# Kernel tuning notes

Measured on AMD Instinct MI355X. Metric: run time of the kernel, lower is better.

The kernel has to match this reference:

```python
import jax, jax.numpy as jnp
import numpy as np

N_NODES = 100000
N_EDGES = 3200000
N_GRAPHS = 1024
HID = 64
NUM_CLASSES = 21


def setup_inputs() -> dict:
    key = jax.random.key(0)
    ks = jax.random.split(key, 12)
    x = jax.random.normal(ks[0], (N_NODES, 1), dtype=jnp.float32)
    edge_index = jax.random.randint(ks[1], (2, N_EDGES), 0, N_NODES, dtype=jnp.int64)
    batch = jnp.sort(jax.random.randint(ks[2], (N_NODES,), 0, N_GRAPHS, dtype=jnp.int64))
    def lin(k, fan_in, fan_out):
        bound = 1.0 / np.sqrt(fan_in)
        return jax.random.uniform(k, (fan_in, fan_out), jnp.float32, -bound, bound)
    return {
        "x": x,
        "edge_index": edge_index,
        "batch": batch,
        # SAGEConv1: lin_l (on aggregated neighbors, with bias), lin_r (root, no bias)
        "W1l": lin(ks[3], 1, HID), "b1": jnp.zeros((HID,), jnp.float32), "W1r": lin(ks[4], 1, HID),
        # SAGEConv2
        "W2l": lin(ks[5], HID, HID), "b2": jnp.zeros((HID,), jnp.float32), "W2r": lin(ks[6], HID, HID),
        # classifier
        "Wc": lin(ks[7], HID, NUM_CLASSES), "bc": jnp.zeros((NUM_CLASSES,), jnp.float32),
    }


def _sage_conv(x, src, dst, Wl, bl, Wr):
    # mean-aggregate neighbor features: gather from src, scatter-mean to dst
    msg = x[src]                                              # [E, F] gather
    agg = jax.ops.segment_sum(msg, dst, num_segments=N_NODES)  # [N, F]
    cnt = jax.ops.segment_sum(jnp.ones((src.shape[0],), x.dtype), dst, num_segments=N_NODES)
    agg = agg / jnp.maximum(cnt, 1.0)[:, None]
    # out = lin_l(aggr) + lin_r(x)
    return agg @ Wl + bl + x @ Wr


def reference(x, edge_index, batch, W1l, b1, W1r, W2l, b2, W2r, Wc, bc):
    src, dst = edge_index[0], edge_index[1]
    h = jax.nn.relu(_sage_conv(x, src, dst, W1l, b1, W1r))
    h = jax.nn.relu(_sage_conv(h, src, dst, W2l, b2, W2r))
    # global mean pool over graphs
    pooled = jax.ops.segment_sum(h, batch, num_segments=N_GRAPHS)
    gcnt = jax.ops.segment_sum(jnp.ones((h.shape[0],), h.dtype), batch, num_segments=N_GRAPHS)
    pooled = pooled / jnp.maximum(gcnt, 1.0)[:, None]
    return pooled @ Wc + bc
```

## Files before the change

### kernel.cpp

```cpp
#include <hip/hip_runtime.h>

#define N_NODES 100000
#define N_EDGES 3200000
#define N_GRAPHS 1024
#define NCLS 21
#define NBKT 782
#define CAP 4480
#define NB 512
#define CHUNK 6250
#define TROW 72

typedef short s8v __attribute__((ext_vector_type(8)));
typedef float f4v __attribute__((ext_vector_type(4)));
typedef float f2v __attribute__((ext_vector_type(2)));

__device__ __forceinline__ float bf2f(unsigned short u) {
    return __uint_as_float(((unsigned)u) << 16);
}
__device__ __forceinline__ unsigned short f2bf(float f) {
    unsigned u = __float_as_uint(f);
    unsigned r = 0x7fffu + ((u >> 16) & 1u);
    return (unsigned short)((u + r) >> 16);
}
__device__ __forceinline__ f2v up2(unsigned w) {
    f2v r;
    r.x = __uint_as_float(w << 16);
    r.y = __uint_as_float(w & 0xffff0000u);
    return r;
}

__global__ void k_prep(const float* __restrict__ W2l, const float* __restrict__ W2r,
                       unsigned short* __restrict__ wp,
                       const int* __restrict__ batch, int* __restrict__ gstart,
                       int* __restrict__ gcur) {
    if (blockIdx.x < 32) {
        int tid = blockIdx.x * 256 + threadIdx.x;
        int frag = tid >> 9;
        int r = tid & 511;
        int L = r >> 3, j = r & 7;
        int kstep = frag >> 2, nt = frag & 3;
        int k = kstep * 32 + (L >> 4) * 8 + j;
        int n = nt * 16 + (L & 15);
        float val = (k < 64) ? W2l[k * 64 + n] : W2r[(k - 64) * 64 + n];
        wp[tid] = f2bf(val);
    } else if (blockIdx.x < 37) {
        int g = (blockIdx.x - 32) * 256 + threadIdx.x;
        if (g > N_GRAPHS) return;
        if (g == N_GRAPHS) { gstart[N_GRAPHS] = N_NODES; return; }
        int lo = 0, hi = N_NODES;
        while (lo < hi) { int m = (lo + hi) >> 1; if (batch[m] < g) lo = m + 1; else hi = m; }
        gstart[g] = lo;
    } else {
        for (int i = threadIdx.x; i < NBKT; i += 256) gcur[i] = i * CAP;
    }
}

__global__ __launch_bounds__(256) void k_binone(const int* __restrict__ src,
                                                const int* __restrict__ dst,
                                                int* __restrict__ gcur,
                                                unsigned int* __restrict__ bins) {
    __shared__ unsigned int ebuf[CHUNK];
    __shared__ unsigned short bbuf[CHUNK];
    __shared__ int lh[NBKT];
    __shared__ int lbase[NBKT];
    int t = threadIdx.x;
    for (int i = t; i < NBKT; i += 256) lh[i] = 0;
    __syncthreads();
    const int2* s2 = (const int2*)(src + blockIdx.x * CHUNK);
    const int2* d2 = (const int2*)(dst + blockIdx.x * CHUNK);
    for (int i = t; i < CHUNK / 2; i += 256) {
        int2 s = s2[i];
        int2 d = d2[i];
        uint2 pp;
        pp.x = ((unsigned)s.x << 7) | (unsigned)(d.x & 127);
        pp.y = ((unsigned)s.y << 7) | (unsigned)(d.y & 127);
        *(uint2*)(&ebuf[2 * i]) = pp;
        bbuf[2 * i]     = (unsigned short)(d.x >> 7);
        bbuf[2 * i + 1] = (unsigned short)(d.y >> 7);
        atomicAdd(&lh[d.x >> 7], 1);
        atomicAdd(&lh[d.y >> 7], 1);
    }
    __syncthreads();
    for (int i = t; i < NBKT; i += 256)
        lbase[i] = atomicAdd(&gcur[i], lh[i]);
    __syncthreads();
    for (int i = t; i < NBKT; i += 256) lh[i] = lbase[i];
    __syncthreads();
    for (int i = t; i < CHUNK; i += 256) {
        int b = (int)bbuf[i];
        int pos = atomicAdd(&lh[b], 1);
        if (pos < (b + 1) * CAP) bins[pos] = ebuf[i];
    }
}

__global__ __launch_bounds__(256) void k_build(
    const int* __restrict__ gcur, unsigned int* __restrict__ bins,
    int* __restrict__ row, unsigned short* __restrict__ deg,
    const float* __restrict__ x,
    const float* __restrict__ W1l, const float* __restrict__ b1,
    const float* __restrict__ W1r, unsigned short* __restrict__ h1b) {
    __shared__ unsigned int ebuf[CAP];
    __shared__ int hist[128];
    __shared__ int curs[128];
    __shared__ int lds[128];
    __shared__ float t1[128];
    int k = blockIdx.x, t = threadIdx.x;
    int e0 = k * CAP;
    int cnt = min(gcur[k] - e0, CAP);
    if (t < 128) { hist[t] = 0; t1[t] = 0.0f; }
    __syncthreads();
    for (int i = t; i < cnt; i += 256) {
        unsigned p = bins[e0 + i];
        ebuf[i] = p;
        atomicAdd(&hist[p & 127u], 1);
    }
    __syncthreads();
    if (t < 128) lds[t] = hist[t];
    __syncthreads();
    for (int off = 1; off < 128; off <<= 1) {
        int cur = (t < 128) ? lds[t] : 0;
        int add = (t < 128 && t >= off) ? lds[t - off] : 0;
        __syncthreads();
        if (t < 128) lds[t] = cur + add;
        __syncthreads();
    }
    if (t < 128) {
        int run = e0 + lds[t] - hist[t];
        curs[t] = run;
        int n = k * 128 + t;
        if (n < N_NODES) { row[n] = run; deg[n] = (unsigned short)hist[t]; }
    }
    __syncthreads();
    for (int i = t; i < cnt; i += 256) {
        unsigned p = ebuf[i];
        int slot = (int)(p & 127u);
        int pos = atomicAdd(&curs[slot], 1);
        bins[pos] = p >> 7;
        atomicAdd(&t1[slot], x[p >> 7]);
    }
    __syncthreads();
    for (int i = t; i < 128 * 64; i += 256) {
        int slot = i >> 6, f = i & 63;
        int n = k * 128 + slot;
        if (n >= N_NODES) break;
        float a = t1[slot] / fmaxf((float)hist[slot], 1.0f);
        float v = a * W1l[f] + b1[f] + x[n] * W1r[f];
        h1b[(size_t)n * 64 + f] = f2bf(fmaxf(v, 0.0f));
    }
}

__global__ __launch_bounds__(256) void k_l2f(
    const int* __restrict__ row, const unsigned short* __restrict__ deg,
    const unsigned int* __restrict__ csr,
    const unsigned short* __restrict__ h1b,
    const unsigned short* __restrict__ wp, const float* __restrict__ b2,
    unsigned short* __restrict__ h2b) {
    __shared__ unsigned short tile[4][16 * TROW];
    int wid = threadIdx.x >> 6;
    int w = blockIdx.x * 4 + wid;
    if (w >= N_NODES / 16) return;
    int L = threadIdx.x & 63;
    int fo = L & 7;
    int g  = L >> 3;
    unsigned short* tw = tile[wid];

    int nA = w * 16 + g;
    int nB = nA + 8;
    int r0A = row[nA]; int dnA = (int)deg[nA];
    int r0B = row[nB]; int dnB = (int)deg[nB];

#define SWZ(v, j) __builtin_amdgcn_ds_swizzle((v), (((j) << 5) | 0x18))
#define GA(j, dj) { int sj = SWZ(idx, j); \
                    dj = *(const uint4*)(h1b + (size_t)(unsigned)sj * 64 + fo * 8); }
#define AC(dj) { p0 += up2(dj.x); p1 += up2(dj.y); p2 += up2(dj.z); p3 += up2(dj.w); }
#define REM(j) if ((j) < rem) { int sj = SWZ(idx, j); \
                    uint4 d = *(const uint4*)(h1b + (size_t)(unsigned)sj * 64 + fo * 8); \
                    AC(d) }

#pragma unroll
    for (int pass = 0; pass < 2; pass++) {
        int r0 = pass ? r0B : r0A;
        int dn = pass ? dnB : dnA;
        int trow = g + 8 * pass;
        int r1 = r0 + dn;
        f2v p0 = {0.f, 0.f}, p1 = p0, p2 = p0, p3 = p0;
        int base = r0;
        int idx = (int)csr[min(base + fo, r1 - 1)];
        while (base + 8 <= r1) {
            int nb = base + 8;
            int idxn = (int)csr[min(nb + fo, r1 - 1)];
            uint4 d0, d1, d2, d3, d4, d5, d6, d7;
            GA(0, d0) GA(1, d1) GA(2, d2) GA(3, d3)
            GA(4, d4) GA(5, d5) GA(6, d6) GA(7, d7)
            idx = idxn;
            AC(d0) AC(d1) AC(d2) AC(d3)
            AC(d4) AC(d5) AC(d6) AC(d7)
            base = nb;
        }
        int rem = r1 - base;
        if (rem > 0) {
            REM(0) REM(1) REM(2) REM(3)
            REM(4) REM(5) REM(6) REM(7)
        }
        float inv = 1.0f / fmaxf((float)dn, 1.0f);
        p0 *= inv; p1 *= inv; p2 *= inv; p3 *= inv;
        unsigned w0 = (unsigned)f2bf(p0.x) | ((unsigned)f2bf(p0.y) << 16);
        unsigned w1 = (unsigned)f2bf(p1.x) | ((unsigned)f2bf(p1.y) << 16);
        unsigned w2 = (unsigned)f2bf(p2.x) | ((unsigned)f2bf(p2.y) << 16);
        unsigned w3 = (unsigned)f2bf(p3.x) | ((unsigned)f2bf(p3.y) << 16);
        uint4 pk; pk.x = w0; pk.y = w1; pk.z = w2; pk.w = w3;
        *(uint4*)(tw + trow * TROW + fo * 8) = pk;
    }
#undef SWZ
#undef GA
#undef AC
#undef REM

    int m = L & 15, q = L >> 4;
    int nrow = w * 16 + m;

    const s8v a0 = *(const s8v*)(tw + m * TROW + q * 8);
    const s8v a1 = *(const s8v*)(tw + m * TROW + 32 + q * 8);
    const s8v a2 = *(const s8v*)(h1b + (size_t)nrow * 64 + q * 8);
    const s8v a3 = *(const s8v*)(h1b + (size_t)nrow * 64 + 32 + q * 8);

#define LOADB(i) s8v B##i = *(const s8v*)(wp + (i) * 512 + L * 8)
    LOADB(0); LOADB(1); LOADB(2); LOADB(3);
    LOADB(4); LOADB(5); LOADB(6); LOADB(7);
    LOADB(8); LOADB(9); LOADB(10); LOADB(11);
    LOADB(12); LOADB(13); LOADB(14); LOADB(15);
#undef LOADB

    f4v acc0 = {0.f, 0.f, 0.f, 0.f}, acc1 = acc0, acc2 = acc0, acc3 = acc0;
    acc0 = __builtin_amdgcn_mfma_f32_16x16x32_bf16(a0, B0,  acc0, 0, 0, 0);
    acc0 = __builtin_amdgcn_mfma_f32_16x16x32_bf16(a1, B4,  acc0, 0, 0, 0);
    acc0 = __builtin_amdgcn_mfma_f32_16x16x32_bf16(a2, B8,  acc0, 0, 0, 0);
    acc0 = __builtin_amdgcn_mfma_f32_16x16x32_bf16(a3, B12, acc0, 0, 0, 0);
    acc1 = __builtin_amdgcn_mfma_f32_16x16x32_bf16(a0, B1,  acc1, 0, 0, 0);
    acc1 = __builtin_amdgcn_mfma_f32_16x16x32_bf16(a1, B5,  acc1, 0, 0, 0);
    acc1 = __builtin_amdgcn_mfma_f32_16x16x32_bf16(a2, B9,  acc1, 0, 0, 0);
    acc1 = __builtin_amdgcn_mfma_f32_16x16x32_bf16(a3, B13, acc1, 0, 0, 0);
    acc2 = __builtin_amdgcn_mfma_f32_16x16x32_bf16(a0, B2,  acc2, 0, 0, 0);
    acc2 = __builtin_amdgcn_mfma_f32_16x16x32_bf16(a1, B6,  acc2, 0, 0, 0);
    acc2 = __builtin_amdgcn_mfma_f32_16x16x32_bf16(a2, B10, acc2, 0, 0, 0);
    acc2 = __builtin_amdgcn_mfma_f32_16x16x32_bf16(a3, B14, acc2, 0, 0, 0);
    acc3 = __builtin_amdgcn_mfma_f32_16x16x32_bf16(a0, B3,  acc3, 0, 0, 0);
    acc3 = __builtin_amdgcn_mfma_f32_16x16x32_bf16(a1, B7,  acc3, 0, 0, 0);
    acc3 = __builtin_amdgcn_mfma_f32_16x16x32_bf16(a2, B11, acc3, 0, 0, 0);
    acc3 = __builtin_amdgcn_mfma_f32_16x16x32_bf16(a3, B15, acc3, 0, 0, 0);

    int fcol = L & 15;
    float bia0 = b2[fcol], bia1 = b2[16 + fcol], bia2 = b2[32 + fcol], bia3 = b2[48 + fcol];
    int rbase = w * 16 + q * 4;
#pragma unroll
    for (int r = 0; r < 4; r++) {
        size_t o = (size_t)(rbase + r) * 64 + fcol;
        h2b[o]      = f2bf(fmaxf(acc0[r] + bia0, 0.0f));
        h2b[o + 16] = f2bf(fmaxf(acc1[r] + bia1, 0.0f));
        h2b[o + 32] = f2bf(fmaxf(acc2[r] + bia2, 0.0f));
        h2b[o + 48] = f2bf(fmaxf(acc3[r] + bia3, 0.0f));
    }
}

__global__ __launch_bounds__(256) void k_head(
    const unsigned short* __restrict__ h2b, const int* __restrict__ gstart,
    const float* __restrict__ Wc, const float* __restrict__ bc,
    float* __restrict__ out) {
    __shared__ float part[4][64];
    __shared__ float rowv[64];
    int g = blockIdx.x;
    int wid = threadIdx.x >> 6;
    int f = threadIdx.x & 63;
    int ns = gstart[g], ne = gstart[g + 1];
    float s = 0.0f;
    int n = ns + wid;
    for (; n + 12 < ne; n += 16) {
        float v0 = bf2f(h2b[(size_t)(n)      * 64 + f]);
        float v1 = bf2f(h2b[(size_t)(n + 4)  * 64 + f]);
        float v2 = bf2f(h2b[(size_t)(n + 8)  * 64 + f]);
        float v3 = bf2f(h2b[(size_t)(n + 12) * 64 + f]);
        s += (v0 + v1) + (v2 + v3);
    }
    for (; n < ne; n += 4) s += bf2f(h2b[(size_t)n * 64 + f]);
    part[wid][f] = s;
    __syncthreads();
    if (threadIdx.x < 64) {
        float tot = part[0][f] + part[1][f] + part[2][f] + part[3][f];
        rowv[f] = tot / fmaxf((float)(ne - ns), 1.0f);
    }
    __syncthreads();
    if (threadIdx.x < NCLS) {
        float acc = bc[threadIdx.x];
#pragma unroll
        for (int kk = 0; kk < 64; kk++) acc += rowv[kk] * Wc[kk * NCLS + threadIdx.x];
        out[g * NCLS + threadIdx.x] = acc;
    }
}

extern "C" void kernel_launch(void* const* d_in, const int* in_sizes, int n_in,
                              void* d_out, int out_size, void* d_ws, size_t ws_size,
                              hipStream_t stream) {
    const float* x     = (const float*)d_in[0];
    const int*   eidx  = (const int*)d_in[1];
    const int*   batch = (const int*)d_in[2];
    const float* W1l   = (const float*)d_in[3];
    const float* b1    = (const float*)d_in[4];
    const float* W1r   = (const float*)d_in[5];
    const float* W2l   = (const float*)d_in[6];
    const float* b2    = (const float*)d_in[7];
    const float* W2r   = (const float*)d_in[8];
    const float* Wc    = (const float*)d_in[9];
    const float* bc    = (const float*)d_in[10];
    float* out = (float*)d_out;

    const int* src = eidx;
    const int* dst = eidx + N_EDGES;

    char* p = (char*)d_ws;
    unsigned int* bins  = (unsigned int*)p;     p += (size_t)NBKT * CAP * 4;
    unsigned short* h1b = (unsigned short*)p;   p += (size_t)N_NODES * 64 * 2;
    unsigned short* h2b = (unsigned short*)p;   p += (size_t)N_NODES * 64 * 2;
    int* row   = (int*)p;                       p += (size_t)(N_NODES + 1) * 4;
    unsigned short* deg = (unsigned short*)p;   p += (size_t)N_NODES * 2;
    int* gcur  = (int*)p;                       p += NBKT * 4;
    int* gstart= (int*)p;                       p += (N_GRAPHS + 1) * 4;
    unsigned short* wp = (unsigned short*)p;    p += 8192 * 2;

    k_prep  <<<38, 256, 0, stream>>>(W2l, W2r, wp, batch, gstart, gcur);
    k_binone<<<NB, 256, 0, stream>>>(src, dst, gcur, bins);
    k_build <<<NBKT, 256, 0, stream>>>(gcur, bins, row, deg, x, W1l, b1, W1r, h1b);
    k_l2f   <<<(N_NODES / 16 + 3) / 4, 256, 0, stream>>>(row, deg, bins, h1b, wp, b2, h2b);
    k_head  <<<N_GRAPHS, 256, 0, stream>>>(h2b, gstart, Wc, bc, out);
}
```

Before: 234.1 us.

## Recompute layer-1 features on the fly from per-node scalars instead of gathering h1

Layer 1 has input dimension 1, so each h1 row is fully determined by two scalars: the mean neighbor x and the node's own x. k_build now stores only these as a float2 per node, and k_l2f rebuilds relu(a*W1l + x*W1r + b1) per edge in registers. The 128-byte bf16 gather per edge becomes an 8-byte gather plus about 64 FMAs and maxes per edge. Using fp32 inputs also drops one bf16 rounding before aggregation. The cost is much more ALU work per edge in exchange for far less gather traffic.

```diff
diff --git a/kernel.cpp b/kernel.cpp
--- a/kernel.cpp
+++ b/kernel.cpp
@@ -22,11 +22,8 @@
     unsigned r = 0x7fffu + ((u >> 16) & 1u);
     return (unsigned short)((u + r) >> 16);
 }
-__device__ __forceinline__ f2v up2(unsigned w) {
-    f2v r;
-    r.x = __uint_as_float(w << 16);
-    r.y = __uint_as_float(w & 0xffff0000u);
-    return r;
+__device__ __forceinline__ f2v max2(f2v v) {
+    f2v r; r.x = fmaxf(v.x, 0.0f); r.y = fmaxf(v.y, 0.0f); return r;
 }
 
 __global__ void k_prep(const float* __restrict__ W2l, const float* __restrict__ W2r,
@@ -96,9 +93,7 @@
 __global__ __launch_bounds__(256) void k_build(
     const int* __restrict__ gcur, unsigned int* __restrict__ bins,
     int* __restrict__ row, unsigned short* __restrict__ deg,
-    const float* __restrict__ x,
-    const float* __restrict__ W1l, const float* __restrict__ b1,
-    const float* __restrict__ W1r, unsigned short* __restrict__ h1b) {
+    const float* __restrict__ x, float2* __restrict__ ax) {
     __shared__ unsigned int ebuf[CAP];
     __shared__ int hist[128];
     __shared__ int curs[128];
@@ -139,20 +134,22 @@
         atomicAdd(&t1[slot], x[p >> 7]);
     }
     __syncthreads();
-    for (int i = t; i < 128 * 64; i += 256) {
-        int slot = i >> 6, f = i & 63;
-        int n = k * 128 + slot;
-        if (n >= N_NODES) break;
-        float a = t1[slot] / fmaxf((float)hist[slot], 1.0f);
-        float v = a * W1l[f] + b1[f] + x[n] * W1r[f];
-        h1b[(size_t)n * 64 + f] = f2bf(fmaxf(v, 0.0f));
+    if (t < 128) {
+        int n = k * 128 + t;
+        if (n < N_NODES) {
+            float a = t1[t] / fmaxf((float)hist[t], 1.0f);
+            float2 v; v.x = a; v.y = x[n];
+            ax[n] = v;
+        }
     }
 }
 
 __global__ __launch_bounds__(256) void k_l2f(
     const int* __restrict__ row, const unsigned short* __restrict__ deg,
     const unsigned int* __restrict__ csr,
-    const unsigned short* __restrict__ h1b,
+    const float2* __restrict__ ax,
+    const float* __restrict__ W1l, const float* __restrict__ b1,
+    const float* __restrict__ W1r,
     const unsigned short* __restrict__ wp, const float* __restrict__ b2,
     unsigned short* __restrict__ h2b) {
     __shared__ unsigned short tile[4][16 * TROW];
@@ -164,18 +161,32 @@
     int g  = L >> 3;
     unsigned short* tw = tile[wid];
 
+    f2v w1l_[4], w1r_[4], bb_[4];
+    {
+        const f2v* pl = (const f2v*)(W1l + fo * 8);
+        const f2v* pr = (const f2v*)(W1r + fo * 8);
+        const f2v* pb = (const f2v*)(b1  + fo * 8);
+#pragma unroll
+        for (int q = 0; q < 4; q++) { w1l_[q] = pl[q]; w1r_[q] = pr[q]; bb_[q] = pb[q]; }
+    }
+
     int nA = w * 16 + g;
     int nB = nA + 8;
     int r0A = row[nA]; int dnA = (int)deg[nA];
     int r0B = row[nB]; int dnB = (int)deg[nB];
 
 #define SWZ(v, j) __builtin_amdgcn_ds_swizzle((v), (((j) << 5) | 0x18))
-#define GA(j, dj) { int sj = SWZ(idx, j); \
-                    dj = *(const uint4*)(h1b + (size_t)(unsigned)sj * 64 + fo * 8); }
-#define AC(dj) { p0 += up2(dj.x); p1 += up2(dj.y); p2 += up2(dj.z); p3 += up2(dj.w); }
-#define REM(j) if ((j) < rem) { int sj = SWZ(idx, j); \
-                    uint4 d = *(const uint4*)(h1b + (size_t)(unsigned)sj * 64 + fo * 8); \
-                    AC(d) }
+#define EDGE(j) { \
+    unsigned au = (unsigned)SWZ((int)__float_as_uint(pr0.x), j); \
+    unsigned xu = (unsigned)SWZ((int)__float_as_uint(pr0.y), j); \
+    float a_ = __uint_as_float(au), x_ = __uint_as_float(xu); \
+    f2v av; av.x = a_; av.y = a_; \
+    f2v xv; xv.x = x_; xv.y = x_; \
+    pp0 += max2(av * w1l_[0] + (xv * w1r_[0] + bb_[0])); \
+    pp1 += max2(av * w1l_[1] + (xv * w1r_[1] + bb_[1])); \
+    pp2 += max2(av * w1l_[2] + (xv * w1r_[2] + bb_[2])); \
+    pp3 += max2(av * w1l_[3] + (xv * w1r_[3] + bb_[3])); }
+#define REM(j) if ((j) < rem) EDGE(j)
 
 #pragma unroll
     for (int pass = 0; pass < 2; pass++) {
@@ -183,19 +194,20 @@
         int dn = pass ? dnB : dnA;
         int trow = g + 8 * pass;
         int r1 = r0 + dn;
-        f2v p0 = {0.f, 0.f}, p1 = p0, p2 = p0, p3 = p0;
+        f2v pp0 = {0.f, 0.f}, pp1 = pp0, pp2 = pp0, pp3 = pp0;
         int base = r0;
-        int idx = (int)csr[min(base + fo, r1 - 1)];
+        int c0 = max(min(base + fo, r1 - 1), r0);
+        unsigned i0 = min((unsigned)csr[c0], (unsigned)(N_NODES - 1));
+        float2 pr0 = ax[i0];
+        int c1 = max(min(base + 8 + fo, r1 - 1), r0);
+        unsigned i1 = min((unsigned)csr[c1], (unsigned)(N_NODES - 1));
         while (base + 8 <= r1) {
-            int nb = base + 8;
-            int idxn = (int)csr[min(nb + fo, r1 - 1)];
-            uint4 d0, d1, d2, d3, d4, d5, d6, d7;
-            GA(0, d0) GA(1, d1) GA(2, d2) GA(3, d3)
-            GA(4, d4) GA(5, d5) GA(6, d6) GA(7, d7)
-            idx = idxn;
-            AC(d0) AC(d1) AC(d2) AC(d3)
-            AC(d4) AC(d5) AC(d6) AC(d7)
-            base = nb;
+            float2 prn = ax[i1];
+            int c2 = max(min(base + 16 + fo, r1 - 1), r0);
+            unsigned i2 = min((unsigned)csr[c2], (unsigned)(N_NODES - 1));
+            EDGE(0) EDGE(1) EDGE(2) EDGE(3)
+            EDGE(4) EDGE(5) EDGE(6) EDGE(7)
+            pr0 = prn; i1 = i2; base += 8;
         }
         int rem = r1 - base;
         if (rem > 0) {
@@ -203,17 +215,17 @@
             REM(4) REM(5) REM(6) REM(7)
         }
         float inv = 1.0f / fmaxf((float)dn, 1.0f);
-        p0 *= inv; p1 *= inv; p2 *= inv; p3 *= inv;
-        unsigned w0 = (unsigned)f2bf(p0.x) | ((unsigned)f2bf(p0.y) << 16);
-        unsigned w1 = (unsigned)f2bf(p1.x) | ((unsigned)f2bf(p1.y) << 16);
-        unsigned w2 = (unsigned)f2bf(p2.x) | ((unsigned)f2bf(p2.y) << 16);
-        unsigned w3 = (unsigned)f2bf(p3.x) | ((unsigned)f2bf(p3.y) << 16);
+        f2v iv; iv.x = inv; iv.y = inv;
+        pp0 *= iv; pp1 *= iv; pp2 *= iv; pp3 *= iv;
+        unsigned w0 = (unsigned)f2bf(pp0.x) | ((unsigned)f2bf(pp0.y) << 16);
+        unsigned w1 = (unsigned)f2bf(pp1.x) | ((unsigned)f2bf(pp1.y) << 16);
+        unsigned w2 = (unsigned)f2bf(pp2.x) | ((unsigned)f2bf(pp2.y) << 16);
+        unsigned w3 = (unsigned)f2bf(pp3.x) | ((unsigned)f2bf(pp3.y) << 16);
         uint4 pk; pk.x = w0; pk.y = w1; pk.z = w2; pk.w = w3;
         *(uint4*)(tw + trow * TROW + fo * 8) = pk;
     }
 #undef SWZ
-#undef GA
-#undef AC
+#undef EDGE
 #undef REM
 
     int m = L & 15, q = L >> 4;
@@ -221,8 +233,28 @@
 
     const s8v a0 = *(const s8v*)(tw + m * TROW + q * 8);
     const s8v a1 = *(const s8v*)(tw + m * TROW + 32 + q * 8);
-    const s8v a2 = *(const s8v*)(h1b + (size_t)nrow * 64 + q * 8);
-    const s8v a3 = *(const s8v*)(h1b + (size_t)nrow * 64 + 32 + q * 8);
+
+    float2 axn = ax[nrow];
+    union { s8v v; unsigned u[4]; } A2, A3;
+    {
+        const f2v* l1 = (const f2v*)(W1l + q * 8);
+        const f2v* r1p = (const f2v*)(W1r + q * 8);
+        const f2v* bp = (const f2v*)(b1 + q * 8);
+        const f2v* l2 = (const f2v*)(W1l + 32 + q * 8);
+        const f2v* r2p = (const f2v*)(W1r + 32 + q * 8);
+        const f2v* b2p = (const f2v*)(b1 + 32 + q * 8);
+        f2v av; av.x = axn.x; av.y = axn.x;
+        f2v xv; xv.x = axn.y; xv.y = axn.y;
+#pragma unroll
+        for (int k = 0; k < 4; k++) {
+            f2v v1 = max2(av * l1[k] + (xv * r1p[k] + bp[k]));
+            f2v v2 = max2(av * l2[k] + (xv * r2p[k] + b2p[k]));
+            A2.u[k] = (unsigned)f2bf(v1.x) | ((unsigned)f2bf(v1.y) << 16);
+            A3.u[k] = (unsigned)f2bf(v2.x) | ((unsigned)f2bf(v2.y) << 16);
+        }
+    }
+    const s8v a2 = A2.v;
+    const s8v a3 = A3.v;
 
 #define LOADB(i) s8v B##i = *(const s8v*)(wp + (i) * 512 + L * 8)
     LOADB(0); LOADB(1); LOADB(2); LOADB(3);
@@ -318,7 +350,7 @@
 
     char* p = (char*)d_ws;
     unsigned int* bins  = (unsigned int*)p;     p += (size_t)NBKT * CAP * 4;
-    unsigned short* h1b = (unsigned short*)p;   p += (size_t)N_NODES * 64 * 2;
+    float2* ax          = (float2*)p;           p += (size_t)N_NODES * 8;
     unsigned short* h2b = (unsigned short*)p;   p += (size_t)N_NODES * 64 * 2;
     int* row   = (int*)p;                       p += (size_t)(N_NODES + 1) * 4;
     unsigned short* deg = (unsigned short*)p;   p += (size_t)N_NODES * 2;
@@ -328,7 +360,8 @@
 
     k_prep  <<<38, 256, 0, stream>>>(W2l, W2r, wp, batch, gstart, gcur);
     k_binone<<<NB, 256, 0, stream>>>(src, dst, gcur, bins);
-    k_build <<<NBKT, 256, 0, stream>>>(gcur, bins, row, deg, x, W1l, b1, W1r, h1b);
-    k_l2f   <<<(N_NODES / 16 + 3) / 4, 256, 0, stream>>>(row, deg, bins, h1b, wp, b2, h2b);
+    k_build <<<NBKT, 256, 0, stream>>>(gcur, bins, row, deg, x, ax);
+    k_l2f   <<<(N_NODES / 16 + 3) / 4, 256, 0, stream>>>(row, deg, bins, ax,
+                                                          W1l, b1, W1r, wp, b2, h2b);
     k_head  <<<N_GRAPHS, 256, 0, stream>>>(h2b, gstart, Wc, bc, out);
 }
```

Measured after the change: 208.4 us. 11.0% less time.
